# Kernel tuning notes

Hardware: AMD Instinct MI355X
Metric: run time of the kernel (lower is better)

The kernel has to match this reference:

```python
import jax, jax.numpy as jnp
import numpy as np

BLOCK = 32      # block_size
KB = 128        # K // BLOCK (mask rows)
NB = 128        # N // BLOCK (mask cols)
DENSITY = 0.1


def _make_mask_indices():
    rng = np.random.RandomState(0)
    mask = rng.rand(KB, NB) < DENSITY
    # guarantee no fully-empty output column (kernel writes zeros there anyway,
    # segment_sum also yields zeros, so this is only to keep stats sane)
    ii, jj = np.nonzero(mask)   # row-major order == torch.nonzero(mask)
    return ii.astype(np.int32), jj.astype(np.int32)


def setup_inputs() -> dict:
    key = jax.random.key(0)
    k1, k2 = jax.random.split(key)
    ii, jj = _make_mask_indices()
    nnz = ii.shape[0]
    M = 4096
    K = KB * BLOCK
    x = jax.random.normal(k1, (M, K), dtype=jnp.float32)
    # block-sparse weight: one [BLOCK, BLOCK] tile per nonzero mask entry,
    # stored in row-major nonzero order (matches torch.nonzero ordering)
    w = jax.random.normal(k2, (nnz, BLOCK, BLOCK), dtype=jnp.float32) * 0.02
    return {"x": x, "w": w, "idx_i": jnp.asarray(ii), "idx_j": jnp.asarray(jj)}


def reference(x, w, idx_i, idx_j):
    # y[:, j*B:(j+1)*B] += x[:, i*B:(i+1)*B] @ w[blk] for each nonzero block (i, j)
    M, K = x.shape
    nnz, B, _ = w.shape
    xb = x.reshape(M, K // B, B)[:, idx_i, :]                 # [M, nnz, B] gather
    partial = jnp.einsum('mnk,nkj->nmj', xb, w)               # [nnz, M, B]
    yb = jax.ops.segment_sum(partial, idx_j, num_segments=NB)  # [NB, M, B] scatter-add
    return yb.transpose(1, 0, 2).reshape(M, NB * B)           # [M, N]
```

## Files before the change

kernel.cpp:

```cpp
#include <hip/hip_runtime.h>
#include <hip/hip_bf16.h>

typedef __bf16 bf16x8 __attribute__((ext_vector_type(8)));
typedef __bf16 bf16x4 __attribute__((ext_vector_type(4)));
typedef float f32x4 __attribute__((ext_vector_type(4)));

#define KDIM 4096
#define NDIM 4096
#define NBJ  128
#define KB   128

__global__ __launch_bounds__(256) void k_prep(
    const float* __restrict__ x, const float* __restrict__ w,
    const int* __restrict__ idx_i, const int* __restrict__ idx_j,
    __bf16* __restrict__ xb, __bf16* __restrict__ wT,
    int* __restrict__ colptr, int* __restrict__ colinfo,
    int nnz, int M, int nbCvt) {
    __shared__ char smem[2176];
    int b = blockIdx.x, t = threadIdx.x;

    if (b < nbCvt) {
        int i  = b & (KB - 1);
        int m0 = (b >> 7) * 64;
        int q  = t & 3, r = t >> 2;
        const float* xp = x + (size_t)(m0 + r) * KDIM + i * 32 + q * 8;
        float4 u = ((const float4*)xp)[0];
        float4 v = ((const float4*)xp)[1];
        bf16x8 o;
        o[0]=(__bf16)u.x; o[1]=(__bf16)u.y; o[2]=(__bf16)u.z; o[3]=(__bf16)u.w;
        o[4]=(__bf16)v.x; o[5]=(__bf16)v.y; o[6]=(__bf16)v.z; o[7]=(__bf16)v.w;
        *(bf16x8*)(xb + ((size_t)i * M + m0 + r) * 32 + q * 8) = o;
    } else if (b < nbCvt + nnz) {
        auto tile = (__bf16(*)[33])smem;
        int n = b - nbCvt;
        float4 v = ((const float4*)(w + (size_t)n * 1024))[t];
        int e = t * 4, k = e >> 5, c = e & 31;
        tile[k][c + 0] = (__bf16)v.x; tile[k][c + 1] = (__bf16)v.y;
        tile[k][c + 2] = (__bf16)v.z; tile[k][c + 3] = (__bf16)v.w;
        __syncthreads();
        int f = t * 4, cc = f >> 5, kk = f & 31;
        bf16x4 o;
        o[0] = tile[kk + 0][cc]; o[1] = tile[kk + 1][cc];
        o[2] = tile[kk + 2][cc]; o[3] = tile[kk + 3][cc];
        ((bf16x4*)(wT + (size_t)n * 1024))[t] = o;
    } else {
        int* cnt = (int*)smem;
        int* cur = cnt + NBJ;
        if (t < NBJ) cnt[t] = 0;
        __syncthreads();
        for (int n = t; n < nnz; n += 256) atomicAdd(&cnt[idx_j[n]], 1);
        __syncthreads();
        int mycount = (t < NBJ) ? cnt[t] : 0;
        for (int off = 1; off < NBJ; off <<= 1) {
            int add = (t < NBJ && t >= off) ? cnt[t - off] : 0;
            __syncthreads();
            if (t < NBJ) cnt[t] += add;
            __syncthreads();
        }
        if (t < NBJ) {
            colptr[t + 1] = cnt[t];
            cur[t] = cnt[t] - mycount;
            if (t == 0) colptr[0] = 0;
        }
        __syncthreads();
        for (int n = t; n < nnz; n += 256) {
            int j = idx_j[n];
            int pos = atomicAdd(&cur[j], 1);
            colinfo[pos] = (idx_i[n] << 16) | n;
        }
    }
}

struct Frag { bf16x8 a0, a1, a2, a3, b0, b1; };

#define MFMA8(F)                                                               \
    acc[0][0] = __builtin_amdgcn_mfma_f32_16x16x32_bf16(F.a0, F.b0, acc[0][0], 0, 0, 0); \
    acc[0][1] = __builtin_amdgcn_mfma_f32_16x16x32_bf16(F.a0, F.b1, acc[0][1], 0, 0, 0); \
    acc[1][0] = __builtin_amdgcn_mfma_f32_16x16x32_bf16(F.a1, F.b0, acc[1][0], 0, 0, 0); \
    acc[1][1] = __builtin_amdgcn_mfma_f32_16x16x32_bf16(F.a1, F.b1, acc[1][1], 0, 0, 0); \
    acc[2][0] = __builtin_amdgcn_mfma_f32_16x16x32_bf16(F.a2, F.b0, acc[2][0], 0, 0, 0); \
    acc[2][1] = __builtin_amdgcn_mfma_f32_16x16x32_bf16(F.a2, F.b1, acc[2][1], 0, 0, 0); \
    acc[3][0] = __builtin_amdgcn_mfma_f32_16x16x32_bf16(F.a3, F.b0, acc[3][0], 0, 0, 0); \
    acc[3][1] = __builtin_amdgcn_mfma_f32_16x16x32_bf16(F.a3, F.b1, acc[3][1], 0, 0, 0);

__global__ __launch_bounds__(256) void k_bsmm(
    const __bf16* __restrict__ xb, const __bf16* __restrict__ wT,
    const int* __restrict__ colptr, const int* __restrict__ colinfo,
    float* __restrict__ y, int M) {
    int RCH = M >> 8;
    int l = blockIdx.x;
    int rc, j;
    if ((RCH & 7) == 0) {
        int rps = RCH >> 3;
        int s = l & 7, u = l >> 3;
        rc = s * rps + (u >> 7);
        j  = u & (NBJ - 1);
    } else {
        rc = l % RCH; j = l / RCH;
    }
    int lane = threadIdx.x & 63, wave = threadIdx.x >> 6;
    int quad = lane >> 4, l16 = lane & 15;
    int wrow = rc * 256 + wave * 64;

    int beg = colptr[j], end = colptr[j + 1];
    int cnt = end - beg;

    f32x4 acc[4][2] = {};

    if (cnt > 0) {
        size_t strideA = (size_t)M * 32;
        const __bf16* xbase = xb + (size_t)(wrow + l16) * 32 + quad * 8;
        const __bf16* wbase = wT + l16 * 32 + quad * 8;
        int cap = cnt - 1;

        if (cnt <= 64) {
            int einfo = colinfo[beg + (lane <= cap ? lane : cap)];
            auto fetch = [&](int p) {
                int pp = p <= cap ? p : cap;
                int ee = __shfl(einfo, pp);
                int n = ee & 0xFFFF, ib = ee >> 16;
                Frag f;
                const __bf16* xp = xbase + (size_t)ib * strideA;
                f.a0 = *(const bf16x8*)(xp);
                f.a1 = *(const bf16x8*)(xp + 16 * 32);
                f.a2 = *(const bf16x8*)(xp + 32 * 32);
                f.a3 = *(const bf16x8*)(xp + 48 * 32);
                const __bf16* wp = wbase + (size_t)n * 1024;
                f.b0 = *(const bf16x8*)(wp);
                f.b1 = *(const bf16x8*)(wp + 512);
                return f;
            };
            Frag f0 = fetch(0);
            Frag f1 = fetch(1);
            Frag f2 = fetch(2);
            int p = 0;
            for (; p + 3 <= cnt; p += 3) {
                MFMA8(f0); f0 = fetch(p + 3);
                MFMA8(f1); f1 = fetch(p + 4);
                MFMA8(f2); f2 = fetch(p + 5);
            }
            if (p < cnt)     { MFMA8(f0); }
            if (p + 1 < cnt) { MFMA8(f1); }
            if (p + 2 < cnt) { MFMA8(f2); }
        } else {
            auto fetch = [&](int p) {
                int pp = p <= cap ? p : cap;
                int ee = colinfo[beg + pp];
                int n = ee & 0xFFFF, ib = ee >> 16;
                Frag f;
                const __bf16* xp = xbase + (size_t)ib * strideA;
                f.a0 = *(const bf16x8*)(xp);
                f.a1 = *(const bf16x8*)(xp + 16 * 32);
                f.a2 = *(const bf16x8*)(xp + 32 * 32);
                f.a3 = *(const bf16x8*)(xp + 48 * 32);
                const __bf16* wp = wbase + (size_t)n * 1024;
                f.b0 = *(const bf16x8*)(wp);
                f.b1 = *(const bf16x8*)(wp + 512);
                return f;
            };
            Frag f0 = fetch(0);
            Frag f1 = fetch(1);
            Frag f2 = fetch(2);
            int p = 0;
            for (; p + 3 <= cnt; p += 3) {
                MFMA8(f0); f0 = fetch(p + 3);
                MFMA8(f1); f1 = fetch(p + 4);
                MFMA8(f2); f2 = fetch(p + 5);
            }
            if (p < cnt)     { MFMA8(f0); }
            if (p + 1 < cnt) { MFMA8(f1); }
            if (p + 2 < cnt) { MFMA8(f2); }
        }
    }

    #pragma unroll
    for (int r = 0; r < 4; ++r)
        #pragma unroll
        for (int ch = 0; ch < 2; ++ch)
            #pragma unroll
            for (int reg = 0; reg < 4; ++reg) {
                int row = wrow + r * 16 + quad * 4 + reg;
                int col = j * 32 + ch * 16 + l16;
                y[(size_t)row * NDIM + col] = acc[r][ch][reg];
            }
}

__global__ __launch_bounds__(256) void k_bsmm_nows(
    const float* __restrict__ x, const float* __restrict__ w,
    const int* __restrict__ idx_i, const int* __restrict__ idx_j,
    float* __restrict__ y, int nnz) {
    __shared__ int list[256];
    __shared__ int listn;
    __shared__ __bf16 tw[32][40];
    int j = blockIdx.y;
    int tid = threadIdx.x;
    int lane = tid & 63, wave = tid >> 6;
    int quad = lane >> 4, l16 = lane & 15;
    int wrow = blockIdx.x * 256 + wave * 64;

    if (tid == 0) listn = 0;
    __syncthreads();
    for (int n = tid; n < nnz; n += 256)
        if (idx_j[n] == j) { int p = atomicAdd(&listn, 1); list[p & 255] = n; }
    __syncthreads();
    int cnt = listn;

    f32x4 acc[4][2] = {};
    for (int p = 0; p < cnt; ++p) {
        int n = list[p];
        int ib = idx_i[n];
        {
            float4 v = ((const float4*)(w + (size_t)n * 1024))[tid];
            int e = tid * 4, k = e >> 5, c = e & 31;
            tw[c + 0][k] = (__bf16)v.x; tw[c + 1][k] = (__bf16)v.y;
            tw[c + 2][k] = (__bf16)v.z; tw[c + 3][k] = (__bf16)v.w;
        }
        __syncthreads();
        bf16x8 a[4];
        #pragma unroll
        for (int r = 0; r < 4; ++r) {
            const float* xp = x + (size_t)(wrow + r * 16 + l16) * KDIM + ib * 32 + quad * 8;
            float4 u = *(const float4*)(xp);
            float4 v = *(const float4*)(xp + 4);
            a[r][0] = (__bf16)u.x; a[r][1] = (__bf16)u.y; a[r][2] = (__bf16)u.z; a[r][3] = (__bf16)u.w;
            a[r][4] = (__bf16)v.x; a[r][5] = (__bf16)v.y; a[r][6] = (__bf16)v.z; a[r][7] = (__bf16)v.w;
        }
        bf16x8 b0 = *(const bf16x8*)&tw[l16][quad * 8];
        bf16x8 b1 = *(const bf16x8*)&tw[l16 + 16][quad * 8];
        #pragma unroll
        for (int r = 0; r < 4; ++r) {
            acc[r][0] = __builtin_amdgcn_mfma_f32_16x16x32_bf16(a[r], b0, acc[r][0], 0, 0, 0);
            acc[r][1] = __builtin_amdgcn_mfma_f32_16x16x32_bf16(a[r], b1, acc[r][1], 0, 0, 0);
        }
        __syncthreads();
    }

    #pragma unroll
    for (int r = 0; r < 4; ++r)
        #pragma unroll
        for (int ch = 0; ch < 2; ++ch)
            #pragma unroll
            for (int reg = 0; reg < 4; ++reg) {
                int row = wrow + r * 16 + quad * 4 + reg;
                int col = j * 32 + ch * 16 + l16;
                y[(size_t)row * NDIM + col] = acc[r][ch][reg];
            }
}

extern "C" void kernel_launch(void* const* d_in, const int* in_sizes, int n_in,
                              void* d_out, int out_size, void* d_ws, size_t ws_size,
                              hipStream_t stream) {
    const float* x     = (const float*)d_in[0];
    const float* w     = (const float*)d_in[1];
    const int*   idx_i = (const int*)d_in[2];
    const int*   idx_j = (const int*)d_in[3];
    float*       y     = (float*)d_out;

    int nnz = in_sizes[2];
    int M   = in_sizes[0] / KDIM;

    size_t xb_bytes = (size_t)M * KDIM * 2;
    size_t wt_bytes = (size_t)nnz * 1024 * 2;
    size_t need = xb_bytes + wt_bytes + (size_t)(NBJ + 2 + nnz) * 4;

    if (ws_size >= need && (M & 255) == 0) {
        __bf16* xb      = (__bf16*)d_ws;
        __bf16* wT      = (__bf16*)((char*)d_ws + xb_bytes);
        int*    colptr  = (int*)((char*)d_ws + xb_bytes + wt_bytes);
        int*    colinfo = colptr + NBJ + 1;
        int nbCvt = KB * (M / 64);
        k_prep<<<nbCvt + nnz + 1, 256, 0, stream>>>(x, w, idx_i, idx_j,
                                                    xb, wT, colptr, colinfo,
                                                    nnz, M, nbCvt);
        k_bsmm<<<(M / 256) * NBJ, 256, 0, stream>>>(xb, wT, colptr, colinfo, y, M);
    } else {
        k_bsmm_nows<<<dim3(M / 256, NBJ), 256, 0, stream>>>(x, w, idx_i, idx_j, y, nnz);
    }
}
```

Measured before the change: 177.2 us.

## Shrink per-block row tile from 256 to 64 rows for more parallelism

Each wave now computes a 16x32 output tile instead of 64x32, so each block covers 64 rows and the grid grows fourfold. Prefetch depth goes from 3 to 4 fragments, and each fragment now carries one A vector instead of four. The aim is higher occupancy and latency hiding, since the accumulators and register footprint are much smaller. The cost is that B tiles are reused across fewer rows, so B loads and colinfo traffic rise and each load feeds fewer MFMAs. The rc swizzle still holds because RCH stays a multiple of 8.

```diff
diff --git a/kernel.cpp b/kernel.cpp
--- a/kernel.cpp
+++ b/kernel.cpp
@@ -71,23 +71,17 @@
     }
 }
 
-struct Frag { bf16x8 a0, a1, a2, a3, b0, b1; };
-
-#define MFMA8(F)                                                               \
-    acc[0][0] = __builtin_amdgcn_mfma_f32_16x16x32_bf16(F.a0, F.b0, acc[0][0], 0, 0, 0); \
-    acc[0][1] = __builtin_amdgcn_mfma_f32_16x16x32_bf16(F.a0, F.b1, acc[0][1], 0, 0, 0); \
-    acc[1][0] = __builtin_amdgcn_mfma_f32_16x16x32_bf16(F.a1, F.b0, acc[1][0], 0, 0, 0); \
-    acc[1][1] = __builtin_amdgcn_mfma_f32_16x16x32_bf16(F.a1, F.b1, acc[1][1], 0, 0, 0); \
-    acc[2][0] = __builtin_amdgcn_mfma_f32_16x16x32_bf16(F.a2, F.b0, acc[2][0], 0, 0, 0); \
-    acc[2][1] = __builtin_amdgcn_mfma_f32_16x16x32_bf16(F.a2, F.b1, acc[2][1], 0, 0, 0); \
-    acc[3][0] = __builtin_amdgcn_mfma_f32_16x16x32_bf16(F.a3, F.b0, acc[3][0], 0, 0, 0); \
-    acc[3][1] = __builtin_amdgcn_mfma_f32_16x16x32_bf16(F.a3, F.b1, acc[3][1], 0, 0, 0);
+struct Frag { bf16x8 a, b0, b1; };
+
+#define MFMA2(F)                                                               \
+    acc0 = __builtin_amdgcn_mfma_f32_16x16x32_bf16(F.a, F.b0, acc0, 0, 0, 0);  \
+    acc1 = __builtin_amdgcn_mfma_f32_16x16x32_bf16(F.a, F.b1, acc1, 0, 0, 0);
 
 __global__ __launch_bounds__(256) void k_bsmm(
     const __bf16* __restrict__ xb, const __bf16* __restrict__ wT,
     const int* __restrict__ colptr, const int* __restrict__ colinfo,
     float* __restrict__ y, int M) {
-    int RCH = M >> 8;
+    int RCH = M >> 6;
     int l = blockIdx.x;
     int rc, j;
     if ((RCH & 7) == 0) {
@@ -100,12 +94,12 @@
     }
     int lane = threadIdx.x & 63, wave = threadIdx.x >> 6;
     int quad = lane >> 4, l16 = lane & 15;
-    int wrow = rc * 256 + wave * 64;
+    int wrow = rc * 64 + wave * 16;
 
     int beg = colptr[j], end = colptr[j + 1];
     int cnt = end - beg;
 
-    f32x4 acc[4][2] = {};
+    f32x4 acc0 = {}, acc1 = {};
 
     if (cnt > 0) {
         size_t strideA = (size_t)M * 32;
@@ -120,11 +114,7 @@
                 int ee = __shfl(einfo, pp);
                 int n = ee & 0xFFFF, ib = ee >> 16;
                 Frag f;
-                const __bf16* xp = xbase + (size_t)ib * strideA;
-                f.a0 = *(const bf16x8*)(xp);
-                f.a1 = *(const bf16x8*)(xp + 16 * 32);
-                f.a2 = *(const bf16x8*)(xp + 32 * 32);
-                f.a3 = *(const bf16x8*)(xp + 48 * 32);
+                f.a  = *(const bf16x8*)(xbase + (size_t)ib * strideA);
                 const __bf16* wp = wbase + (size_t)n * 1024;
                 f.b0 = *(const bf16x8*)(wp);
                 f.b1 = *(const bf16x8*)(wp + 512);
@@ -133,26 +123,25 @@
             Frag f0 = fetch(0);
             Frag f1 = fetch(1);
             Frag f2 = fetch(2);
+            Frag f3 = fetch(3);
             int p = 0;
-            for (; p + 3 <= cnt; p += 3) {
-                MFMA8(f0); f0 = fetch(p + 3);
-                MFMA8(f1); f1 = fetch(p + 4);
-                MFMA8(f2); f2 = fetch(p + 5);
+            for (; p + 4 <= cnt; p += 4) {
+                MFMA2(f0); f0 = fetch(p + 4);
+                MFMA2(f1); f1 = fetch(p + 5);
+                MFMA2(f2); f2 = fetch(p + 6);
+                MFMA2(f3); f3 = fetch(p + 7);
             }
-            if (p < cnt)     { MFMA8(f0); }
-            if (p + 1 < cnt) { MFMA8(f1); }
-            if (p + 2 < cnt) { MFMA8(f2); }
+            if (p < cnt)     { MFMA2(f0); }
+            if (p + 1 < cnt) { MFMA2(f1); }
+            if (p + 2 < cnt) { MFMA2(f2); }
+            if (p + 3 < cnt) { MFMA2(f3); }
         } else {
             auto fetch = [&](int p) {
                 int pp = p <= cap ? p : cap;
                 int ee = colinfo[beg + pp];
                 int n = ee & 0xFFFF, ib = ee >> 16;
                 Frag f;
-                const __bf16* xp = xbase + (size_t)ib * strideA;
-                f.a0 = *(const bf16x8*)(xp);
-                f.a1 = *(const bf16x8*)(xp + 16 * 32);
-                f.a2 = *(const bf16x8*)(xp + 32 * 32);
-                f.a3 = *(const bf16x8*)(xp + 48 * 32);
+                f.a  = *(const bf16x8*)(xbase + (size_t)ib * strideA);
                 const __bf16* wp = wbase + (size_t)n * 1024;
                 f.b0 = *(const bf16x8*)(wp);
                 f.b1 = *(const bf16x8*)(wp + 512);
@@ -161,28 +150,27 @@
             Frag f0 = fetch(0);
             Frag f1 = fetch(1);
             Frag f2 = fetch(2);
+            Frag f3 = fetch(3);
             int p = 0;
-            for (; p + 3 <= cnt; p += 3) {
-                MFMA8(f0); f0 = fetch(p + 3);
-                MFMA8(f1); f1 = fetch(p + 4);
-                MFMA8(f2); f2 = fetch(p + 5);
+            for (; p + 4 <= cnt; p += 4) {
+                MFMA2(f0); f0 = fetch(p + 4);
+                MFMA2(f1); f1 = fetch(p + 5);
+                MFMA2(f2); f2 = fetch(p + 6);
+                MFMA2(f3); f3 = fetch(p + 7);
             }
-            if (p < cnt)     { MFMA8(f0); }
-            if (p + 1 < cnt) { MFMA8(f1); }
-            if (p + 2 < cnt) { MFMA8(f2); }
+            if (p < cnt)     { MFMA2(f0); }
+            if (p + 1 < cnt) { MFMA2(f1); }
+            if (p + 2 < cnt) { MFMA2(f2); }
+            if (p + 3 < cnt) { MFMA2(f3); }
         }
     }
 
     #pragma unroll
-    for (int r = 0; r < 4; ++r)
-        #pragma unroll
-        for (int ch = 0; ch < 2; ++ch)
-            #pragma unroll
-            for (int reg = 0; reg < 4; ++reg) {
-                int row = wrow + r * 16 + quad * 4 + reg;
-                int col = j * 32 + ch * 16 + l16;
-                y[(size_t)row * NDIM + col] = acc[r][ch][reg];
-            }
+    for (int reg = 0; reg < 4; ++reg) {
+        int row = wrow + quad * 4 + reg;
+        y[(size_t)row * NDIM + j * 32 + l16]      = acc0[reg];
+        y[(size_t)row * NDIM + j * 32 + 16 + l16] = acc1[reg];
+    }
 }
 
 __global__ __launch_bounds__(256) void k_bsmm_nows(
@@ -272,7 +260,7 @@
         k_prep<<<nbCvt + nnz + 1, 256, 0, stream>>>(x, w, idx_i, idx_j,
                                                     xb, wT, colptr, colinfo,
                                                     nnz, M, nbCvt);
-        k_bsmm<<<(M / 256) * NBJ, 256, 0, stream>>>(xb, wT, colptr, colinfo, y, M);
+        k_bsmm<<<(M / 64) * NBJ, 256, 0, stream>>>(xb, wT, colptr, colinfo, y, M);
     } else {
         k_bsmm_nows<<<dim3(M / 256, NBJ), 256, 0, stream>>>(x, w, idx_i, idx_j, y, nnz);
     }
```

Result: slower. 221.8 us (+25.2%).
